# Kernel optimization log

Measured on AMD Instinct MI355X. Metric: run time of the kernel, lower is better.

## Reference

```python
import jax, jax.numpy as jnp
import numpy as np

H = 128; R = 8; VN = 100; VA = 64
N = 8192; B = 64; L = 48; E = 65536


def setup_inputs() -> dict:
    key = jax.random.key(0)
    ks = jax.random.split(key, 24)
    s = 0.05
    nodeTypes = jax.random.randint(ks[0], (N,), 0, VN)
    edge_index = jax.random.randint(ks[1], (2, E), 0, N)
    edge_attr = jax.random.randint(ks[2], (E,), 0, R)
    bs = jnp.repeat(jnp.arange(B), N // B)              # sorted node->graph map
    nodes_bs = jnp.full((B,), N // B, dtype=jnp.int32)  # nodes per graph
    len_seq = jax.random.randint(ks[3], (B,), 1, L + 1).at[0].set(L)  # max == L
    sequence_input = (jax.random.uniform(ks[4], (N, L)) < 0.05).astype(jnp.float32)
    action_input = jax.random.randint(ks[5], (B,), 0, VA)
    params = dict(
        emb_nodes=jax.random.normal(ks[6], (VN, H)) * s,
        emb_actions=jax.random.normal(ks[7], (VA, H)) * s,
        rgcn_rel=jax.random.normal(ks[8], (3, R, H, H)) * s,   # per-layer relation weights
        rgcn_root=jax.random.normal(ks[9], (3, H, H)) * s,
        rgcn_bias=jnp.zeros((3, H)),
        gru_w_ih=jax.random.normal(ks[10], (3 * H, H)) * s,
        gru_w_hh=jax.random.normal(ks[11], (3 * H, H)) * s,
        gru_b_ih=jnp.zeros((3 * H,)),
        gru_b_hh=jnp.zeros((3 * H,)),
        linA_w=jax.random.normal(ks[12], (H, H)) * s,
        linA_b=jnp.zeros((H,)),
        linAf_w=jax.random.normal(ks[13], (VA, H)) * s,
        linAf_b=jnp.zeros((VA,)),
        linN_w=jax.random.normal(ks[14], (H, 2 * H)) * s,
        linN_b=jnp.zeros((H,)),
        linNf_w=jax.random.normal(ks[15], (1, H)) * s,
        linNf_b=jnp.zeros((1,)),
    )
    return dict(nodeTypes=nodeTypes, edge_index=edge_index, edge_attr=edge_attr,
                bs=bs, nodes_bs=nodes_bs, len_seq=len_seq,
                sequence_input=sequence_input, action_input=action_input, **params)


def reference(nodeTypes, edge_index, edge_attr, bs, nodes_bs, len_seq,
              sequence_input, action_input,
              emb_nodes, emb_actions, rgcn_rel, rgcn_root, rgcn_bias,
              gru_w_ih, gru_w_hh, gru_b_ih, gru_b_hh,
              linA_w, linA_b, linAf_w, linAf_b,
              linN_w, linN_b, linNf_w, linNf_b):
    n = nodeTypes.shape[0]
    b = nodes_bs.shape[0]
    h = emb_nodes.shape[1]
    r = rgcn_rel.shape[1]
    l = sequence_input.shape[1]

    x = emb_nodes[nodeTypes]                               # [N,H]
    src, dst = edge_index[0], edge_index[1]
    seg = dst * r + edge_attr                              # per (target, relation) segment
    cnt = jax.ops.segment_sum(jnp.ones((src.shape[0],), x.dtype), seg, n * r)
    denom = jnp.maximum(cnt, 1.0).reshape(n, r, 1)
    for li in range(3):
        agg = jax.ops.segment_sum(x[src], seg, n * r).reshape(n, r, h) / denom
        x = jax.nn.relu(jnp.einsum('nrh,rho->no', agg, rgcn_rel[li])
                        + x @ rgcn_root[li] + rgcn_bias[li])

    # global mean pool -> graph embedding
    h_G = jax.ops.segment_sum(x, bs, b) / nodes_bs[:, None].astype(x.dtype)  # [B,H]
    action = jax.nn.relu(h_G @ linA_w.T + linA_b) @ linAf_w.T + linAf_b      # [B,VA]

    sos = emb_actions[action_input][:, None, :]            # [B,1,H]
    # sequence embeddings: sum over nodes in each graph of seq[i,t]*x[i]
    emb_seq = sequence_input[:, :, None] * x[:, None, :]   # [N,L,H]
    out = jax.ops.segment_sum(emb_seq, bs, b)              # [B,L,H]
    input_gru = jnp.concatenate([sos, out], axis=1)[:, :l] # packed GRU only sees first L steps

    # single-layer GRU, h0 = h_G (torch gate order r,z,n)
    xW = input_gru @ gru_w_ih.T + gru_b_ih                 # [B,L,3H]
    def step(hprev, xw):
        hW = hprev @ gru_w_hh.T + gru_b_hh
        xr, xz, xn = jnp.split(xw, 3, -1)
        hr, hz, hn = jnp.split(hW, 3, -1)
        rg = jax.nn.sigmoid(xr + hr)
        zg = jax.nn.sigmoid(xz + hz)
        ng = jnp.tanh(xn + rg * hn)
        hnew = (1.0 - zg) * ng + zg * hprev
        return hnew, hnew
    _, hs = jax.lax.scan(step, h_G, jnp.swapaxes(xW, 0, 1))
    seq_out = jnp.swapaxes(hs, 0, 1)                       # [B,L,H]
    mask = jnp.arange(l)[None, :] < len_seq[:, None]       # pad_packed zero-pads
    seq_out = seq_out * mask[:, :, None]

    out_gru = seq_out[bs]                                  # repeat_interleave -> [N,L,H]
    concats = jnp.concatenate(
        [out_gru, jnp.broadcast_to(x[:, None, :], (n, l, h))], axis=2)  # [N,L,2H]
    hid = jax.nn.relu(concats @ linN_w.T + linN_b)         # [N,L,H]
    logits = (hid @ linNf_w.T + linNf_b)[..., 0]           # [N,L]

    # scatter_softmax over nodes grouped by graph (dim 0)
    m = jax.lax.stop_gradient(jax.ops.segment_max(logits, bs, b))
    e = jnp.exp(logits - m[bs])
    ssum = jax.ops.segment_sum(e, bs, b)
    nodes_final = e / ssum[bs]
    return action, nodes_final
```

## Files before the change

### kernel.cpp

```cpp
#include <hip/hip_runtime.h>
#include <hip/hip_bf16.h>

#define H   128
#define RR  8
#define NN  8192
#define BB  64
#define LL  48
#define EE  65536
#define NPG 128
#define VA  64
#define NSEG (NN*RR)

typedef unsigned short u16;
typedef unsigned int   u32;

__device__ __forceinline__ float b2f(u16 u) {
    union { u32 i; float f; } v; v.i = ((u32)u) << 16; return v.f;
}
__device__ __forceinline__ u16 f2b(float f) {
    union { float f; u32 i; } v; v.f = f;
    u32 x = v.i;
    return (u16)((x + 0x7fffu + ((x >> 16) & 1u)) >> 16);
}
__device__ __forceinline__ float2 up2(u32 p) {
    union { u32 i; float f; } a, b;
    a.i = p << 16; b.i = p & 0xffff0000u;
    return make_float2(a.f, b.f);
}
__device__ __forceinline__ u32 pk2(float a, float b) {
    return ((u32)f2b(b) << 16) | (u32)f2b(a);
}
__device__ __forceinline__ float rcpf(float x) { return __builtin_amdgcn_rcpf(x); }

typedef __attribute__((ext_vector_type(8))) short bf16x8;
typedef __attribute__((ext_vector_type(4))) float f32x4;

__global__ __launch_bounds__(256) void k_init(const int* __restrict__ nodeTypes,
                                              const float* __restrict__ emb_nodes,
                                              float* __restrict__ x0,
                                              int* __restrict__ fill) {
    int idx = blockIdx.x * 256 + threadIdx.x;
    if (idx < NSEG) fill[idx] = 0;
    if (idx < NN * H) {
        int n = idx >> 7, h = idx & (H - 1);
        x0[idx] = emb_nodes[(size_t)nodeTypes[n] * H + h];
    }
}

__global__ __launch_bounds__(256) void k_hist(const int* __restrict__ edge_index,
                                              const int* __restrict__ edge_attr,
                                              int* __restrict__ fill) {
    int e = blockIdx.x * 256 + threadIdx.x;
    if (e < EE) {
        int seg = edge_index[EE + e] * RR + edge_attr[e];
        atomicAdd(&fill[seg], 1);
    }
}

__global__ __launch_bounds__(256) void k_scan1(const int* __restrict__ fill,
                                               int* __restrict__ bsum) {
    __shared__ int red[4];
    int tid = threadIdx.x, lane = tid & 63, wv = tid >> 6;
    int v = fill[blockIdx.x * 256 + tid];
#pragma unroll
    for (int off = 32; off >= 1; off >>= 1) v += __shfl_down(v, off, 64);
    if (lane == 0) red[wv] = v;
    __syncthreads();
    if (tid == 0) bsum[blockIdx.x] = red[0] + red[1] + red[2] + red[3];
}

__global__ __launch_bounds__(256) void k_scan2(const int* __restrict__ bsum,
                                               int* __restrict__ boff,
                                               int* __restrict__ rowptr) {
    __shared__ int s[256];
    int tid = threadIdx.x;
    int v0 = bsum[tid];
    s[tid] = v0;
    __syncthreads();
    for (int off = 1; off < 256; off <<= 1) {
        int v = (tid >= off) ? s[tid - off] : 0;
        __syncthreads();
        s[tid] += v;
        __syncthreads();
    }
    boff[tid] = s[tid] - v0;
    if (tid == 255) rowptr[NSEG] = s[255];
}

__global__ __launch_bounds__(256) void k_scan3(const int* __restrict__ boff,
                                               int* __restrict__ fill,
                                               int* __restrict__ rowptr) {
    __shared__ int s[256];
    int tid = threadIdx.x;
    int g = blockIdx.x * 256 + tid;
    int c = fill[g];
    s[tid] = c;
    __syncthreads();
    for (int off = 1; off < 256; off <<= 1) {
        int v = (tid >= off) ? s[tid - off] : 0;
        __syncthreads();
        s[tid] += v;
        __syncthreads();
    }
    int r = boff[blockIdx.x] + s[tid] - c;
    rowptr[g] = r;
    fill[g] = r;
}

__global__ __launch_bounds__(256) void k_scatter(const int* __restrict__ edge_index,
                                                 const int* __restrict__ edge_attr,
                                                 int* __restrict__ fill,
                                                 int* __restrict__ colidx) {
    int e = blockIdx.x * 256 + threadIdx.x;
    if (e < EE) {
        int seg = edge_index[EE + e] * RR + edge_attr[e];
        int pos = atomicAdd(&fill[seg], 1);
        colidx[pos] = edge_index[e];
    }
}

__global__ __launch_bounds__(256) void k_wprep(const float* __restrict__ rel,
                                               const float* __restrict__ root,
                                               const float* __restrict__ w_ih,
                                               u16* __restrict__ WTt,
                                               u16* __restrict__ WTih,
                                               float* __restrict__ hGsum) {
    int idx = blockIdx.x * 256 + threadIdx.x;
    if (idx < 384 * H) WTih[idx] = f2b(w_ih[idx]);
    if (idx < BB * H) hGsum[idx] = 0.f;
    if (idx >= 3 * 147456) return;
    int li  = idx / 147456;
    int rem = idx - li * 147456;
    int tile = rem / 36864;
    int r2   = rem - tile * 36864;
    int ks   = r2 / 1024;
    int r3   = r2 - ks * 1024;
    int sub  = r3 >> 9;
    int r4   = r3 & 511;
    int lane = r4 >> 3, j = r4 & 7;
    int col = tile * 32 + sub * 16 + (lane & 15);
    int k   = ks * 32 + (lane >> 4) * 8 + j;
    float v;
    if (k < 1024) v = rel[(((size_t)li * RR + (k >> 7)) * H + (k & 127)) * H + col];
    else          v = root[((size_t)li * H + (k - 1024)) * H + col];
    WTt[idx] = f2b(v);
}

#define RGN 16
#define EPRE 512

__global__ __launch_bounds__(256) void k_rgcn(const float* __restrict__ xin,
                                              float* __restrict__ xout,
                                              const u16* __restrict__ WTt,
                                              const float* __restrict__ bias,
                                              const int* __restrict__ rowptr,
                                              const int* __restrict__ colidx,
                                              float* __restrict__ hGsum) {
    __shared__ u32 ab[RGN * 580];
    __shared__ int begs[RGN * RR + 1];
    __shared__ int eidx[EPRE];
    int tid = threadIdx.x, wv = tid >> 6, lane = tid & 63;
    int n0 = blockIdx.x * RGN, segbase = n0 * RR;

    if (tid <= RGN * RR) begs[tid] = rowptr[segbase + tid];
    __syncthreads();
    int E0 = begs[0], ne = begs[RGN * RR] - E0;
    for (int i = tid; i < ne && i < EPRE; i += 256) eidx[i] = colidx[E0 + i];
    __syncthreads();

    for (int s = wv; s < RGN * RR; s += 4) {
        int beg = begs[s], end = begs[s + 1];
        float a0 = 0.f, a1 = 0.f;
        for (int e = beg; e < end; ++e) {
            int off = e - E0;
            int src = (off < EPRE) ? eidx[off] : colidx[e];
            float2 v = ((const float2*)(xin + (size_t)src * H))[lane];
            a0 += v.x; a1 += v.y;
        }
        float inv = 1.f / fmaxf((float)(end - beg), 1.f);
        ab[(s >> 3) * 580 + ((s & 7) << 6) + lane] = pk2(a0 * inv, a1 * inv);
    }
    for (int i = wv; i < RGN; i += 4) {
        const float* xr = xin + (size_t)(n0 + i) * H + 2 * lane;
        ab[i * 580 + 512 + lane] = pk2(xr[0], xr[1]);
    }
    __syncthreads();

    int m = lane & 15, quad = lane >> 4;
    int colbase = wv * 32;
    const u32* aP = ab + m * 580 + quad * 4;
    const u32* bT = (const u32*)WTt + (size_t)wv * 36 * 512 + lane * 4;
    f32x4 acc0 = {0.f, 0.f, 0.f, 0.f}, acc1 = {0.f, 0.f, 0.f, 0.f};
    bf16x8 b0c = *(const bf16x8*)bT;
    bf16x8 b1c = *(const bf16x8*)(bT + 256);
    for (int ks = 0; ks < 36; ++ks) {
        bf16x8 b0n, b1n;
        if (ks < 35) {
            b0n = *(const bf16x8*)(bT + (ks + 1) * 512);
            b1n = *(const bf16x8*)(bT + (ks + 1) * 512 + 256);
        }
        bf16x8 a = *(const bf16x8*)(aP + ks * 16);
        acc0 = __builtin_amdgcn_mfma_f32_16x16x32_bf16(a, b0c, acc0, 0, 0, 0);
        acc1 = __builtin_amdgcn_mfma_f32_16x16x32_bf16(a, b1c, acc1, 0, 0, 0);
        b0c = b0n; b1c = b1n;
    }
    int c0 = colbase + m, c1 = c0 + 16;
    float bv0 = bias[c0], bv1 = bias[c1];
    float so0 = 0.f, so1 = 0.f;
#pragma unroll
    for (int rg = 0; rg < 4; ++rg) {
        int n = n0 + quad * 4 + rg;
        float o0 = fmaxf(acc0[rg] + bv0, 0.f);
        float o1 = fmaxf(acc1[rg] + bv1, 0.f);
        xout[(size_t)n * H + c0] = o0;
        xout[(size_t)n * H + c1] = o1;
        so0 += o0; so1 += o1;
    }
    if (hGsum) {
        so0 += __shfl_xor(so0, 16, 64);
        so0 += __shfl_xor(so0, 32, 64);
        so1 += __shfl_xor(so1, 16, 64);
        so1 += __shfl_xor(so1, 32, 64);
        if (quad == 0) {
            int g = n0 >> 7;
            atomicAdd(&hGsum[g * H + c0], so0);
            atomicAdd(&hGsum[g * H + c1], so1);
        }
    }
}

__global__ __launch_bounds__(128) void k_pool_act(const float* __restrict__ hGsum,
                                                  const int* __restrict__ nodes_bs,
                                                  const float* __restrict__ linA_w,
                                                  const float* __restrict__ linA_b,
                                                  const float* __restrict__ linAf_w,
                                                  const float* __restrict__ linAf_b,
                                                  float* __restrict__ hG,
                                                  float* __restrict__ out) {
    __shared__ float hgs[H], t1[H];
    int b = blockIdx.x, h = threadIdx.x;
    float hg = hGsum[(size_t)b * H + h] / (float)nodes_bs[b];
    hG[(size_t)b * H + h] = hg;
    hgs[h] = hg;
    __syncthreads();
    float acc = linA_b[h];
    const float* wr = linA_w + (size_t)h * H;
    for (int k = 0; k < H; ++k) acc += wr[k] * hgs[k];
    t1[h] = fmaxf(acc, 0.f);
    __syncthreads();
    if (h < VA) {
        float a = linAf_b[h];
        const float* w2 = linAf_w + (size_t)h * H;
        for (int k = 0; k < H; ++k) a += w2[k] * t1[k];
        out[(size_t)b * VA + h] = a;
    }
}

__global__ __launch_bounds__(256) void k_seqpool(const float* __restrict__ xf,
                                                 const float* __restrict__ seq,
                                                 const float* __restrict__ emb_actions,
                                                 const int* __restrict__ action_input,
                                                 float* __restrict__ igG) {
    __shared__ float xg[64][H];
    __shared__ u16 lists[LL][64];
    __shared__ int cnts[LL];
    int b = blockIdx.x, tid = threadIdx.x;
    int col = tid & 127, tg = tid >> 7;
    float acc[24];
#pragma unroll
    for (int m = 0; m < 24; ++m) acc[m] = 0.f;

    for (int chunk = 0; chunk < 2; ++chunk) {
        int i0 = b * NPG + chunk * 64;
        __syncthreads();
        if (tid < LL) cnts[tid] = 0;
        __syncthreads();
        for (int idx = tid; idx < 64 * H / 4; idx += 256)
            ((float4*)&xg[0][0])[idx] = ((const float4*)(xf + (size_t)i0 * H))[idx];
        for (int idx = tid; idx < 64 * LL; idx += 256) {
            int i = idx / LL, t = idx - i * LL;
            if (seq[(size_t)(i0 + i) * LL + t] != 0.f) {
                int p = atomicAdd(&cnts[t], 1);
                lists[t][p] = (u16)i;
            }
        }
        __syncthreads();
        for (int m = 0; m < 24; ++m) {
            int t = tg + 2 * m;
            int c = cnts[t];
            float a = acc[m];
            for (int p = 0; p < c; ++p) a += xg[lists[t][p]][col];
            acc[m] = a;
        }
    }
    if (tid < H)
        igG[((size_t)b * LL) * H + tid] = emb_actions[(size_t)action_input[b] * H + tid];
#pragma unroll
    for (int m = 0; m < 24; ++m) {
        int t = tg + 2 * m;
        if (t < LL - 1)
            igG[((size_t)b * LL + t + 1) * H + col] = acc[m];
    }
}

__global__ __launch_bounds__(256) void k_xw(const float* __restrict__ igG,
                                            const u16* __restrict__ WTih,
                                            const float* __restrict__ b_ih,
                                            u16* __restrict__ xwG) {
    __shared__ u32 ab[16 * 68];
    int tid = threadIdx.x, wv = tid >> 6, lane = tid & 63;
    int n0 = blockIdx.x * 16;
    for (int s = tid; s < 16 * 64; s += 256) {
        int row = s >> 6, kp = s & 63;
        float2 v = *(const float2*)(igG + (size_t)(n0 + row) * H + 2 * kp);
        ab[row * 68 + kp] = pk2(v.x, v.y);
    }
    __syncthreads();
    int m = lane & 15, quad = lane >> 4;
    const u32* aP = ab + m * 68 + quad * 4;
    f32x4 acc[6];
#pragma unroll
    for (int i = 0; i < 6; ++i) acc[i] = (f32x4){0.f, 0.f, 0.f, 0.f};
#pragma unroll
    for (int ks = 0; ks < 4; ++ks) {
        bf16x8 a = *(const bf16x8*)(aP + ks * 16);
#pragma unroll
        for (int tc = 0; tc < 6; ++tc) {
            int colr = wv * 96 + tc * 16 + m;
            bf16x8 bfr = *(const bf16x8*)((const u32*)WTih + (size_t)colr * 64 + quad * 4 + ks * 16);
            acc[tc] = __builtin_amdgcn_mfma_f32_16x16x32_bf16(a, bfr, acc[tc], 0, 0, 0);
        }
    }
#pragma unroll
    for (int tc = 0; tc < 6; ++tc) {
        int c = wv * 96 + tc * 16 + m;
        float bv = b_ih[c];
#pragma unroll
        for (int rg = 0; rg < 4; ++rg) {
            int r = n0 + quad * 4 + rg;
            xwG[(size_t)r * 384 + c] = f2b(acc[tc][rg] + bv);
        }
    }
}

__global__ __launch_bounds__(768) void k_gru(const u16* __restrict__ xwG,
                                             const float* __restrict__ hG,
                                             const float* __restrict__ w_hh,
                                             const float* __restrict__ b_hh,
                                             const int* __restrict__ len_seq,
                                             float* __restrict__ soutG) {
    __shared__ float xws[LL][3 * H];
    __shared__ float souts[LL][H];
    __shared__ float hbuf[H];
    __shared__ float gh[3 * H];
    int b = blockIdx.x, tid = threadIdx.x;

    const u16* src = xwG + (size_t)b * LL * 384;
    float* xf = &xws[0][0];
    for (int idx = tid; idx < LL * 384; idx += 768) xf[idx] = b2f(src[idx]);
    if (tid < H) hbuf[tid] = hG[(size_t)b * H + tid];

    int j = tid >> 1, half = tid & 1;
    u32 wh[32];
    {
        const float* wp = w_hh + (size_t)j * H + 2 * half;
#pragma unroll
        for (int k = 0; k < 32; ++k) wh[k] = pk2(wp[4 * k], wp[4 * k + 1]);
    }
    float bhh = b_hh[j];
    int ls = len_seq[b];
    __syncthreads();

    for (int t = 0; t < LL; ++t) {
        const float* hb = hbuf + 2 * half;
        float p[4] = {0.f, 0.f, 0.f, 0.f};
#pragma unroll
        for (int k = 0; k < 32; ++k) {
            float2 w = up2(wh[k]);
            float2 h2 = *(const float2*)&hb[4 * k];
            p[k & 3] += w.x * h2.x + w.y * h2.y;
        }
        float a = (p[0] + p[1]) + (p[2] + p[3]);
        a += __shfl_xor(a, 1, 64);
        if (half == 0) gh[j] = a + bhh;
        __syncthreads();
        if (tid < H) {
            float rg = rcpf(1.f + __expf(-(xws[t][tid] + gh[tid])));
            float zg = rcpf(1.f + __expf(-(xws[t][tid + H] + gh[tid + H])));
            float u  = xws[t][tid + 2 * H] + rg * gh[tid + 2 * H];
            float ng = 1.f - 2.f * rcpf(__expf(2.f * u) + 1.f);
            float hnew = (1.f - zg) * ng + zg * hbuf[tid];
            hbuf[tid] = hnew;
            souts[t][tid] = hnew;
        }
        __syncthreads();
    }

    for (int idx = tid; idx < LL * H; idx += 768) {
        int t = idx >> 7, hh = idx & 127;
        soutG[((size_t)b * LL + t) * H + hh] = (t < ls) ? souts[t][hh] : 0.f;
    }
}

__global__ __launch_bounds__(256) void k_a2(const float* __restrict__ soutG,
                                            const float* __restrict__ linN_w,
                                            float* __restrict__ A2) {
    __shared__ float wb[32][130];
    __shared__ float xl[16][H];
    int tid = threadIdx.x;
    int n0 = blockIdx.x * 16;
    for (int idx = tid; idx < 16 * H; idx += 256)
        xl[idx >> 7][idx & 127] = soutG[(size_t)n0 * H + idx];
    int col = tid & 127, g = tid >> 7;
    float acc[8] = {0.f, 0.f, 0.f, 0.f, 0.f, 0.f, 0.f, 0.f};
    for (int c = 0; c < 4; ++c) {
        int k0 = c * 32;
        __syncthreads();
        for (int idx = tid; idx < 32 * H; idx += 256) {
            int r = idx >> 5, kk = idx & 31;
            wb[kk][r] = linN_w[(size_t)r * (2 * H) + k0 + kk];
        }
        __syncthreads();
#pragma unroll
        for (int kk = 0; kk < 32; ++kk) {
            float w = wb[kk][col];
#pragma unroll
            for (int j = 0; j < 8; ++j) acc[j] += xl[g * 8 + j][k0 + kk] * w;
        }
    }
#pragma unroll
    for (int j = 0; j < 8; ++j)
        A2[(size_t)(n0 + g * 8 + j) * H + col] = acc[j];
}

__global__ __launch_bounds__(256) void k_bx(const float* __restrict__ xf,
                                            const float* __restrict__ linN_w,
                                            const float* __restrict__ linN_b,
                                            u16* __restrict__ BxU) {
    __shared__ float wb[32][130];
    __shared__ float xl[16][H];
    int tid = threadIdx.x;
    int n0 = blockIdx.x * 16;
    for (int idx = tid; idx < 16 * H; idx += 256)
        xl[idx >> 7][idx & 127] = xf[(size_t)n0 * H + idx];
    int col = tid & 127, g = tid >> 7;
    float bv = linN_b[col];
    float acc[8] = {bv, bv, bv, bv, bv, bv, bv, bv};
    for (int c = 0; c < 4; ++c) {
        int k0 = c * 32;
        __syncthreads();
        for (int idx = tid; idx < 32 * H; idx += 256) {
            int r = idx >> 5, kk = idx & 31;
            wb[kk][r] = linN_w[(size_t)r * (2 * H) + H + k0 + kk];
        }
        __syncthreads();
#pragma unroll
        for (int kk = 0; kk < 32; ++kk) {
            float w = wb[kk][col];
#pragma unroll
            for (int j = 0; j < 8; ++j) acc[j] += xl[g * 8 + j][k0 + kk] * w;
        }
    }
#pragma unroll
    for (int j = 0; j < 8; ++j)
        BxU[(size_t)(n0 + g * 8 + j) * H + col] = f2b(acc[j]);
}

__global__ __launch_bounds__(256) void k_logits(const float* __restrict__ A2,
                                                const u16* __restrict__ BxU,
                                                const float* __restrict__ linNf_w,
                                                float* __restrict__ logits) {
    __shared__ float a2s[LL][130];
    __shared__ float bxs[16][130];
    __shared__ float w2s[H];
    int tid = threadIdx.x;
    int g = blockIdx.x >> 3, tile = blockIdx.x & 7;
    int n0g = g * NPG + tile * 16;

    for (int i2 = tid; i2 < LL * 64; i2 += 256) {
        int r = i2 >> 6, c2 = i2 & 63;
        *(float2*)&a2s[r][2 * c2] = *(const float2*)(A2 + ((size_t)g * LL + r) * H + 2 * c2);
    }
    for (int iu = tid; iu < 16 * 64; iu += 256) {
        int r = iu >> 6, c = iu & 63;
        float2 v = up2(((const u32*)BxU)[(size_t)(n0g + r) * 64 + c]);
        *(float2*)&bxs[r][2 * c] = v;
    }
    if (tid < H) w2s[tid] = linNf_w[tid];
    __syncthreads();

    int n = tid & 15, tt = tid >> 4;
#pragma unroll
    for (int pass = 0; pass < 3; ++pass) {
        int t = tt + 16 * pass;
        float acc = 0.f;
#pragma unroll
        for (int kp = 0; kp < 64; ++kp) {
            float2 a2 = *(const float2*)&a2s[t][2 * kp];
            float2 bx = *(const float2*)&bxs[n][2 * kp];
            float2 w  = *(const float2*)&w2s[2 * kp];
            acc += w.x * fmaxf(a2.x + bx.x, 0.f) + w.y * fmaxf(a2.y + bx.y, 0.f);
        }
        logits[(size_t)(n0g + n) * LL + t] = acc;
    }
}

__global__ __launch_bounds__(256) void k_softmax(const float* __restrict__ logits,
                                                 float* __restrict__ out) {
    __shared__ float lg[NPG][LL + 1];
    __shared__ float pm[4][LL], ps[4][LL];
    __shared__ float mv[LL], inv[LL];
    int b = blockIdx.x, tid = threadIdx.x;
    int n0 = b * NPG;
    for (int idx = tid; idx < NPG * LL; idx += 256) {
        int n = idx / LL, t = idx - n * LL;
        lg[n][t] = logits[(size_t)n0 * LL + idx];
    }
    __syncthreads();
    int t = tid & 63, seg = tid >> 6;
    if (t < LL) {
        float m = -1e30f;
        int nb = seg * 32;
        for (int n = nb; n < nb + 32; ++n) m = fmaxf(m, lg[n][t]);
        pm[seg][t] = m;
    }
    __syncthreads();
    if (tid < LL)
        mv[tid] = fmaxf(fmaxf(pm[0][tid], pm[1][tid]), fmaxf(pm[2][tid], pm[3][tid]));
    __syncthreads();
    if (t < LL) {
        float m = mv[t], s = 0.f;
        int nb = seg * 32;
        for (int n = nb; n < nb + 32; ++n) {
            float e = __expf(lg[n][t] - m);
            lg[n][t] = e;
            s += e;
        }
        ps[seg][t] = s;
    }
    __syncthreads();
    if (tid < LL)
        inv[tid] = 1.f / (ps[0][tid] + ps[1][tid] + ps[2][tid] + ps[3][tid]);
    __syncthreads();
    for (int idx = tid; idx < NPG * LL; idx += 256) {
        int n = idx / LL, tc = idx - n * LL;
        out[(size_t)BB * VA + (size_t)n0 * LL + idx] = lg[n][tc] * inv[tc];
    }
}

extern "C" void kernel_launch(void* const* d_in, const int* in_sizes, int n_in,
                              void* d_out, int out_size, void* d_ws, size_t ws_size,
                              hipStream_t stream) {
    (void)in_sizes; (void)n_in; (void)out_size; (void)ws_size;
    const int*   nodeTypes    = (const int*)d_in[0];
    const int*   edge_index   = (const int*)d_in[1];
    const int*   edge_attr    = (const int*)d_in[2];
    const int*   nodes_bs     = (const int*)d_in[4];
    const int*   len_seq      = (const int*)d_in[5];
    const float* seq_in       = (const float*)d_in[6];
    const int*   action_input = (const int*)d_in[7];
    const float* emb_nodes    = (const float*)d_in[8];
    const float* emb_actions  = (const float*)d_in[9];
    const float* rgcn_rel     = (const float*)d_in[10];
    const float* rgcn_root    = (const float*)d_in[11];
    const float* rgcn_bias    = (const float*)d_in[12];
    const float* gru_w_ih     = (const float*)d_in[13];
    const float* gru_w_hh     = (const float*)d_in[14];
    const float* gru_b_ih     = (const float*)d_in[15];
    const float* gru_b_hh     = (const float*)d_in[16];
    const float* linA_w       = (const float*)d_in[17];
    const float* linA_b       = (const float*)d_in[18];
    const float* linAf_w      = (const float*)d_in[19];
    const float* linAf_b      = (const float*)d_in[20];
    const float* linN_w       = (const float*)d_in[21];
    const float* linN_b       = (const float*)d_in[22];
    const float* linNf_w      = (const float*)d_in[23];

    char* w = (char*)d_ws;
    float* x0      = (float*)(w + 0);
    u16*   xwG     = (u16*)  (w + 0);
    float* logitsW = (float*)(w + 0);
    float* soutG   = (float*)(w + 2359296);
    float* x1      = (float*)(w + 4194304);
    float* igG     = (float*)(w + 8388608);
    float* A2      = (float*)(w + 8388608);
    u16*   BxU     = (u16*)  (w + 9961472);
    int*   bsum    = (int*)  (w + 9961472);
    int*   boff    = (int*)  (w + 9962496);
    float* hGsum   = (float*)(w + 9969664);
    int*   rowptr  = (int*)  (w + 11567104);
    int*   fill    = (int*)  (w + 11829760);
    u16*   WTih    = (u16*)  (w + 11829760);
    float* hG      = (float*)(w + 12058624);
    int*   colidx  = (int*)  (w + 12091904);
    u16*   WT      = (u16*)  (w + 12616192);

    float* out_f = (float*)d_out;

    k_init<<<dim3(4096), dim3(256), 0, stream>>>(nodeTypes, emb_nodes, x0, fill);
    k_hist<<<dim3(256), dim3(256), 0, stream>>>(edge_index, edge_attr, fill);
    k_scan1<<<dim3(256), dim3(256), 0, stream>>>(fill, bsum);
    k_scan2<<<dim3(1), dim3(256), 0, stream>>>(bsum, boff, rowptr);
    k_scan3<<<dim3(256), dim3(256), 0, stream>>>(boff, fill, rowptr);
    k_scatter<<<dim3(256), dim3(256), 0, stream>>>(edge_index, edge_attr, fill, colidx);
    k_wprep<<<dim3(1728), dim3(256), 0, stream>>>(rgcn_rel, rgcn_root, gru_w_ih,
                                                  WT, WTih, hGsum);

    const int rg_grid = NN / RGN;
    k_rgcn<<<dim3(rg_grid), dim3(256), 0, stream>>>(x0, x1,
        WT + 0 * 147456, rgcn_bias + 0 * H, rowptr, colidx, nullptr);
    k_rgcn<<<dim3(rg_grid), dim3(256), 0, stream>>>(x1, x0,
        WT + 1 * 147456, rgcn_bias + 1 * H, rowptr, colidx, nullptr);
    k_rgcn<<<dim3(rg_grid), dim3(256), 0, stream>>>(x0, x1,
        WT + 2 * 147456, rgcn_bias + 2 * H, rowptr, colidx, hGsum);

    k_pool_act<<<dim3(BB), dim3(128), 0, stream>>>(hGsum, nodes_bs, linA_w, linA_b,
                                                   linAf_w, linAf_b, hG, out_f);
    k_seqpool<<<dim3(BB), dim3(256), 0, stream>>>(x1, seq_in, emb_actions, action_input, igG);
    k_xw<<<dim3(BB * LL / 16), dim3(256), 0, stream>>>(igG, WTih, gru_b_ih, xwG);
    k_gru<<<dim3(BB), dim3(768), 0, stream>>>(xwG, hG, gru_w_hh, gru_b_hh, len_seq, soutG);
    k_a2<<<dim3(BB * LL / 16), dim3(256), 0, stream>>>(soutG, linN_w, A2);
    k_bx<<<dim3(NN / 16), dim3(256), 0, stream>>>(x1, linN_w, linN_b, BxU);
    k_logits<<<dim3(BB * 8), dim3(256), 0, stream>>>(A2, BxU, linNf_w, logitsW);
    k_softmax<<<dim3(BB), dim3(256), 0, stream>>>(logitsW, out_f);
}
```

Baseline: 369.6 us.

## Batch GRU recurrence across 16 graphs per block using MFMA

Replaces the one-block-per-graph scalar GRU kernel with a kernel that processes 16 graphs per block. The recurrent h@W_hh product runs on bf16 MFMA with W_hh held in registers and h split into hi/lo bf16 parts for accuracy. k_xw now writes xW in a graph-interleaved layout and folds b_hh for the r/z gates into the bias. The next step's xW is prefetched while the current step computes. Only 4 blocks are launched, so parallelism drops, but each of the 48 serial steps should be much shorter.

Result: slower. 380.4 us (+2.9%).

```diff
diff --git a/kernel.cpp b/kernel.cpp
--- a/kernel.cpp
+++ b/kernel.cpp
@@ -10,6 +10,7 @@
 #define NPG 128
 #define VA  64
 #define NSEG (NN*RR)
+#define GPB 16
 
 typedef unsigned short u16;
 typedef unsigned int   u32;
@@ -34,6 +35,7 @@
 
 typedef __attribute__((ext_vector_type(8))) short bf16x8;
 typedef __attribute__((ext_vector_type(4))) float f32x4;
+typedef __attribute__((ext_vector_type(4))) unsigned short u16x4;
 
 __global__ __launch_bounds__(256) void k_init(const int* __restrict__ nodeTypes,
                                               const float* __restrict__ emb_nodes,
@@ -306,6 +308,7 @@
 __global__ __launch_bounds__(256) void k_xw(const float* __restrict__ igG,
                                             const u16* __restrict__ WTih,
                                             const float* __restrict__ b_ih,
+                                            const float* __restrict__ b_hh,
                                             u16* __restrict__ xwG) {
     __shared__ u32 ab[16 * 68];
     int tid = threadIdx.x, wv = tid >> 6, lane = tid & 63;
@@ -334,71 +337,139 @@
 #pragma unroll
     for (int tc = 0; tc < 6; ++tc) {
         int c = wv * 96 + tc * 16 + m;
-        float bv = b_ih[c];
+        float bv = b_ih[c] + ((c < 256) ? b_hh[c] : 0.f);
 #pragma unroll
         for (int rg = 0; rg < 4; ++rg) {
             int r = n0 + quad * 4 + rg;
-            xwG[(size_t)r * 384 + c] = f2b(acc[tc][rg] + bv);
-        }
-    }
-}
-
-__global__ __launch_bounds__(768) void k_gru(const u16* __restrict__ xwG,
-                                             const float* __restrict__ hG,
-                                             const float* __restrict__ w_hh,
-                                             const float* __restrict__ b_hh,
-                                             const int* __restrict__ len_seq,
-                                             float* __restrict__ soutG) {
-    __shared__ float xws[LL][3 * H];
-    __shared__ float souts[LL][H];
-    __shared__ float hbuf[H];
-    __shared__ float gh[3 * H];
-    int b = blockIdx.x, tid = threadIdx.x;
-
-    const u16* src = xwG + (size_t)b * LL * 384;
-    float* xf = &xws[0][0];
-    for (int idx = tid; idx < LL * 384; idx += 768) xf[idx] = b2f(src[idx]);
-    if (tid < H) hbuf[tid] = hG[(size_t)b * H + tid];
-
-    int j = tid >> 1, half = tid & 1;
-    u32 wh[32];
-    {
-        const float* wp = w_hh + (size_t)j * H + 2 * half;
-#pragma unroll
-        for (int k = 0; k < 32; ++k) wh[k] = pk2(wp[4 * k], wp[4 * k + 1]);
-    }
-    float bhh = b_hh[j];
-    int ls = len_seq[b];
+            int bb = r / 48, tt = r - bb * 48;
+            size_t o = ((size_t)((bb >> 4) * 48 + tt) * GPB + (bb & (GPB - 1))) * 384 + c;
+            xwG[o] = f2b(acc[tc][rg] + bv);
+        }
+    }
+}
+
+__device__ __forceinline__ int heidx(int g, int k) {
+    return (g << 7) + (k ^ ((g & 7) << 3));
+}
+
+__global__ __launch_bounds__(256) void k_gruM(const u16* __restrict__ xw2,
+                                              const float* __restrict__ hG,
+                                              const float* __restrict__ w_hh,
+                                              const float* __restrict__ b_hh,
+                                              const int* __restrict__ len_seq,
+                                              float* __restrict__ soutG) {
+    __shared__ __align__(16) u16 hA[2][2][GPB * H];
+    int tid = threadIdx.x;
+    int lane = tid & 63, wv = tid >> 6;
+    int mi = lane & 15, quad = lane >> 4;
+    int gblk = blockIdx.x;
+    int g_abs = gblk * GPB + mi;
+    int hh1 = 16 * wv + quad * 4;
+    int hh2 = hh1 + 64;
+
+    bf16x8 wfr[6][4];
+#pragma unroll
+    for (int ti = 0; ti < 6; ++ti) {
+        int T = wv + ((ti >> 1) << 3) + ((ti & 1) << 2);
+#pragma unroll
+        for (int ks = 0; ks < 4; ++ks) {
+            const float* wp = w_hh + (size_t)(16 * T + mi) * H + quad * 8 + ks * 32;
+            float4 f0 = *(const float4*)wp;
+            float4 f1 = *(const float4*)(wp + 4);
+            bf16x8 v;
+            v[0] = (short)f2b(f0.x); v[1] = (short)f2b(f0.y);
+            v[2] = (short)f2b(f0.z); v[3] = (short)f2b(f0.w);
+            v[4] = (short)f2b(f1.x); v[5] = (short)f2b(f1.y);
+            v[6] = (short)f2b(f1.z); v[7] = (short)f2b(f1.w);
+            wfr[ti][ks] = v;
+        }
+    }
+    float4 bn0 = *(const float4*)(b_hh + 256 + hh1);
+    float4 bn1 = *(const float4*)(b_hh + 256 + hh2);
+    float4 h0a = *(const float4*)(hG + (size_t)g_abs * H + hh1);
+    float4 h0b = *(const float4*)(hG + (size_t)g_abs * H + hh2);
+    int ls = len_seq[g_abs];
+
+    float hp[2][4]  = {{h0a.x, h0a.y, h0a.z, h0a.w}, {h0b.x, h0b.y, h0b.z, h0b.w}};
+    float bnn[2][4] = {{bn0.x, bn0.y, bn0.z, bn0.w}, {bn1.x, bn1.y, bn1.z, bn1.w}};
+
+    auto storeh = [&](int buf, int hh, const float* hv) {
+        u16x4 hi4, lo4;
+#pragma unroll
+        for (int r = 0; r < 4; ++r) {
+            u16 hi = f2b(hv[r]);
+            hi4[r] = hi;
+            lo4[r] = f2b(hv[r] - b2f(hi));
+        }
+        int e = heidx(mi, hh);
+        *(u16x4*)&hA[buf][0][e] = hi4;
+        *(u16x4*)&hA[buf][1][e] = lo4;
+    };
+    auto loadxw = [&](int t, u16x4* d) {
+        const u16* p = xw2 + (((size_t)gblk * LL + t) * GPB + mi) * 384;
+        d[0] = *(const u16x4*)(p + hh1);
+        d[1] = *(const u16x4*)(p + 128 + hh1);
+        d[2] = *(const u16x4*)(p + 256 + hh1);
+        d[3] = *(const u16x4*)(p + hh2);
+        d[4] = *(const u16x4*)(p + 128 + hh2);
+        d[5] = *(const u16x4*)(p + 256 + hh2);
+    };
+
+    u16x4 xc[6], xnx[6];
+    loadxw(0, xc);
+    storeh(0, hh1, hp[0]);
+    storeh(0, hh2, hp[1]);
     __syncthreads();
 
     for (int t = 0; t < LL; ++t) {
-        const float* hb = hbuf + 2 * half;
-        float p[4] = {0.f, 0.f, 0.f, 0.f};
-#pragma unroll
-        for (int k = 0; k < 32; ++k) {
-            float2 w = up2(wh[k]);
-            float2 h2 = *(const float2*)&hb[4 * k];
-            p[k & 3] += w.x * h2.x + w.y * h2.y;
-        }
-        float a = (p[0] + p[1]) + (p[2] + p[3]);
-        a += __shfl_xor(a, 1, 64);
-        if (half == 0) gh[j] = a + bhh;
-        __syncthreads();
-        if (tid < H) {
-            float rg = rcpf(1.f + __expf(-(xws[t][tid] + gh[tid])));
-            float zg = rcpf(1.f + __expf(-(xws[t][tid + H] + gh[tid + H])));
-            float u  = xws[t][tid + 2 * H] + rg * gh[tid + 2 * H];
-            float ng = 1.f - 2.f * rcpf(__expf(2.f * u) + 1.f);
-            float hnew = (1.f - zg) * ng + zg * hbuf[tid];
-            hbuf[tid] = hnew;
-            souts[t][tid] = hnew;
-        }
-        __syncthreads();
-    }
-
-    for (int idx = tid; idx < LL * H; idx += 768) {
-        int t = idx >> 7, hh = idx & 127;
-        soutG[((size_t)b * LL + t) * H + hh] = (t < ls) ? souts[t][hh] : 0.f;
+        int buf = t & 1;
+        if (t < LL - 1) loadxw(t + 1, xnx);
+        const u16* hHi = &hA[buf][0][0];
+        const u16* hLo = &hA[buf][1][0];
+        f32x4 acc[6];
+        acc[0] = (f32x4){0.f, 0.f, 0.f, 0.f};
+        acc[1] = (f32x4){0.f, 0.f, 0.f, 0.f};
+        acc[2] = (f32x4){0.f, 0.f, 0.f, 0.f};
+        acc[3] = (f32x4){0.f, 0.f, 0.f, 0.f};
+        acc[4] = (f32x4){bnn[0][0], bnn[0][1], bnn[0][2], bnn[0][3]};
+        acc[5] = (f32x4){bnn[1][0], bnn[1][1], bnn[1][2], bnn[1][3]};
+#pragma unroll
+        for (int ks = 0; ks < 4; ++ks) {
+            int e = heidx(mi, quad * 8 + ks * 32);
+            bf16x8 bh = *(const bf16x8*)&hHi[e];
+            bf16x8 bl = *(const bf16x8*)&hLo[e];
+#pragma unroll
+            for (int ti = 0; ti < 6; ++ti) {
+                acc[ti] = __builtin_amdgcn_mfma_f32_16x16x32_bf16(wfr[ti][ks], bh, acc[ti], 0, 0, 0);
+                acc[ti] = __builtin_amdgcn_mfma_f32_16x16x32_bf16(wfr[ti][ks], bl, acc[ti], 0, 0, 0);
+            }
+        }
+#pragma unroll
+        for (int p = 0; p < 2; ++p) {
+            int hh = p ? hh2 : hh1;
+            float hv[4];
+            float4 so;
+#pragma unroll
+            for (int r = 0; r < 4; ++r) {
+                float xr = b2f(xc[3 * p + 0][r]);
+                float xz = b2f(xc[3 * p + 1][r]);
+                float xn = b2f(xc[3 * p + 2][r]);
+                float gr = acc[0 + p][r], gz = acc[2 + p][r], gn = acc[4 + p][r];
+                float rg = rcpf(1.f + __expf(-(xr + gr)));
+                float zg = rcpf(1.f + __expf(-(xz + gz)));
+                float u  = xn + rg * gn;
+                float ng = 1.f - 2.f * rcpf(__expf(2.f * u) + 1.f);
+                float hn = (1.f - zg) * ng + zg * hp[p][r];
+                hp[p][r] = hn;
+                hv[r] = hn;
+                ((float*)&so)[r] = (t < ls) ? hn : 0.f;
+            }
+            *(float4*)(soutG + ((size_t)g_abs * LL + t) * H + hh) = so;
+            storeh(buf ^ 1, hh, hv);
+        }
+#pragma unroll
+        for (int i = 0; i < 6; ++i) xc[i] = xnx[i];
+        __syncthreads();
     }
 }
 
@@ -617,8 +688,9 @@
     k_pool_act<<<dim3(BB), dim3(128), 0, stream>>>(hGsum, nodes_bs, linA_w, linA_b,
                                                    linAf_w, linAf_b, hG, out_f);
     k_seqpool<<<dim3(BB), dim3(256), 0, stream>>>(x1, seq_in, emb_actions, action_input, igG);
-    k_xw<<<dim3(BB * LL / 16), dim3(256), 0, stream>>>(igG, WTih, gru_b_ih, xwG);
-    k_gru<<<dim3(BB), dim3(768), 0, stream>>>(xwG, hG, gru_w_hh, gru_b_hh, len_seq, soutG);
+    k_xw<<<dim3(BB * LL / 16), dim3(256), 0, stream>>>(igG, WTih, gru_b_ih, gru_b_hh, xwG);
+    k_gruM<<<dim3(BB / GPB), dim3(256), 0, stream>>>(xwG, hG, gru_w_hh, gru_b_hh,
+                                                     len_seq, soutG);
     k_a2<<<dim3(BB * LL / 16), dim3(256), 0, stream>>>(soutG, linN_w, A2);
     k_bx<<<dim3(NN / 16), dim3(256), 0, stream>>>(x1, linN_w, linN_b, BxU);
     k_logits<<<dim3(BB * 8), dim3(256), 0, stream>>>(A2, BxU, linNf_w, logitsW);
```
